# Performance work log

Measured on AMD Instinct MI355X. Metric: run time of the kernel, lower is better.

The kernel has to match this reference:

```python
import jax, jax.numpy as jnp
import numpy as np

# Dimensions (match init_kwargs / input_specs)
NF, NLOC, NALL = 1, 1024, 2048
N_DIM, E_DIM, A_DIM = 128, 16, 64
NNEI, A_SEL, AXIS = 120, 20, 4

act = jax.nn.silu


def _lin(key, i, o):
    k1, k2 = jax.random.split(key)
    w = jax.random.normal(k1, (i, o), jnp.float32) / np.float32(np.sqrt(i))
    b = jax.random.normal(k2, (o,), jnp.float32) * 0.01
    return w, b


def setup_inputs() -> dict:
    key = jax.random.key(0)
    ks = jax.random.split(key, 16)
    d = {}
    d["node_ebd_ext"] = jax.random.normal(ks[0], (NF, NALL, N_DIM), jnp.float32)
    d["edge_ebd"] = jax.random.normal(ks[1], (NF, NLOC, NNEI, E_DIM), jnp.float32)
    d["h2"] = jax.random.normal(ks[2], (NF, NLOC, NNEI, 3), jnp.float32)
    d["angle_ebd"] = jax.random.normal(ks[3], (NF, NLOC, A_SEL, A_SEL, A_DIM), jnp.float32)
    d["sw"] = jax.random.uniform(ks[4], (NF, NLOC, NNEI), jnp.float32)
    d["a_sw"] = jax.random.uniform(ks[5], (NF, NLOC, A_SEL), jnp.float32)
    d["nlist"] = jax.random.randint(ks[6], (NF, NLOC, NNEI), 0, NALL)
    d["nlist_mask"] = jnp.ones((NF, NLOC, NNEI), bool)
    d["a_nlist_mask"] = jnp.ones((NF, NLOC, A_SEL), bool)
    edge_info_dim = 2 * N_DIM + E_DIM          # 272
    angle_dim = A_DIM + N_DIM + 2 * E_DIM      # 224 (a_compress_rate == 0)
    d["w_node_self"], d["b_node_self"] = _lin(ks[7], N_DIM, N_DIM)
    d["w_node_sym"], d["b_node_sym"] = _lin(ks[8], (N_DIM + E_DIM) * AXIS, N_DIM)
    d["w_node_edge"], d["b_node_edge"] = _lin(ks[9], edge_info_dim, N_DIM)
    d["w_edge_self"], d["b_edge_self"] = _lin(ks[10], edge_info_dim, E_DIM)
    d["w_ea1"], d["b_ea1"] = _lin(ks[11], angle_dim, E_DIM)
    d["w_ea2"], d["b_ea2"] = _lin(ks[12], E_DIM, E_DIM)
    d["w_angle_self"], d["b_angle_self"] = _lin(ks[13], angle_dim, A_DIM)
    # res_residual update style: one learnable residual scale per update branch,
    # init 'const' with update_residual = 0.1
    d["n_res"] = jnp.full((3, N_DIM), 0.1, jnp.float32)  # self, sym, edge-message
    d["e_res"] = jnp.full((2, E_DIM), 0.1, jnp.float32)  # self, angle-message
    d["a_res"] = jnp.full((1, A_DIM), 0.1, jnp.float32)  # self
    return d


def _forward(node_ebd_ext, edge_ebd, h2, angle_ebd, sw, a_sw,
             w_node_self, b_node_self, w_node_sym, b_node_sym,
             w_node_edge, b_node_edge, w_edge_self, b_edge_self,
             w_ea1, b_ea1, w_ea2, b_ea2, w_angle_self, b_angle_self,
             n_res, e_res, a_res, nlist, nlist_mask, a_nlist_mask):
    nf, nall, n_dim = node_ebd_ext.shape
    _, nloc, nnei, e_dim = edge_ebd.shape
    a_sel = angle_ebd.shape[2]
    node_ebd = node_ebd_ext[:, :nloc]

    # gather neighbor node embeddings: nf x nloc x nnei x n_dim
    nei_node = jax.vmap(lambda tbl, idx: tbl[idx])(node_ebd_ext, nlist)
    nei_node = jnp.where(nlist_mask[..., None], nei_node, 0.0)

    # 1) node self update
    node_self_update = act(node_ebd @ w_node_self + b_node_self)

    # 2) node symmetrization update (grrg over both edge and neighbor-node features)
    wgt = (sw * nlist_mask)[..., None]

    def sym(ebd):
        e = ebd * wgt
        hg = jnp.einsum('flni,flnd->flid', h2, e) / np.float32(nnei)  # f,l,3,d
        grrg = jnp.einsum('flid,flia->flda', hg, hg[..., :AXIS]) / np.float32(3.0)
        return grrg.reshape(nf, nloc, -1)

    node_sym_in = jnp.concatenate([sym(nei_node), sym(edge_ebd)], axis=-1)
    node_sym_update = act(node_sym_in @ w_node_sym + b_node_sym)

    # 3) edge info = [node_i, node_j, edge_ij]
    node_i = jnp.broadcast_to(node_ebd[:, :, None, :], (nf, nloc, nnei, n_dim))
    edge_info = jnp.concatenate([node_i, nei_node, edge_ebd], axis=-1)

    # 3a) node <- edge message (sw-weighted mean over neighbors)
    node_edge_update = act(edge_info @ w_node_edge + b_node_edge) * sw[..., None]
    node_edge_update = node_edge_update.sum(axis=-2) / np.float32(nnei)

    node_new = (node_ebd + n_res[0] * node_self_update
                + n_res[1] * node_sym_update + n_res[2] * node_edge_update)

    # 4) edge self update
    edge_self_update = act(edge_info @ w_edge_self + b_edge_self)

    # 5) angle branch (a_compress_rate == 0)
    edge_for_angle = jnp.where(a_nlist_mask[..., None], edge_ebd[:, :, :a_sel, :], 0.0)
    node_angle = jnp.broadcast_to(node_ebd[:, :, None, None, :], (nf, nloc, a_sel, a_sel, n_dim))
    e_ik = jnp.broadcast_to(edge_for_angle[:, :, :, None, :], (nf, nloc, a_sel, a_sel, e_dim))
    e_ij = jnp.broadcast_to(edge_for_angle[:, :, None, :, :], (nf, nloc, a_sel, a_sel, e_dim))
    angle_info = jnp.concatenate([angle_ebd, node_angle, e_ik, e_ij], axis=-1)

    # edge <- angle message: sw-weighted reduce over one angle axis
    ea = act(angle_info @ w_ea1 + b_ea1)  # nf,nloc,a_sel,a_sel,e_dim
    weighted = a_sw[:, :, :, None, None] * a_sw[:, :, None, :, None] * ea
    reduced = weighted.sum(axis=-2) / np.float32(np.sqrt(a_sel))  # nf,nloc,a_sel,e_dim
    pad = jnp.zeros((nf, nloc, nnei - a_sel, e_dim), edge_ebd.dtype)
    padded = jnp.concatenate([reduced, pad], axis=2)
    full_mask = jnp.concatenate(
        [a_nlist_mask, jnp.zeros((nf, nloc, nnei - a_sel), bool)], axis=-1)
    # smooth_edge_update = False: keep original edge ebd where angle mask is off
    padded = jnp.where(full_mask[..., None], padded, edge_ebd)
    edge_angle_update = act(padded @ w_ea2 + b_ea2)

    edge_new = edge_ebd + e_res[0] * edge_self_update + e_res[1] * edge_angle_update

    # angle self update
    angle_self_update = act(angle_info @ w_angle_self + b_angle_self)
    angle_new = angle_ebd + a_res[0] * angle_self_update

    return node_new, edge_new, angle_new


def reference(node_ebd_ext, edge_ebd, h2, angle_ebd, sw, a_sw, nlist, nlist_mask,
              a_nlist_mask, w_node_self, b_node_self, w_node_sym, b_node_sym,
              w_node_edge, b_node_edge, w_edge_self, b_edge_self, w_ea1, b_ea1,
              w_ea2, b_ea2, w_angle_self, b_angle_self, n_res, e_res, a_res):
    return _forward(node_ebd_ext, edge_ebd, h2, angle_ebd, sw, a_sw,
                    w_node_self, b_node_self, w_node_sym, b_node_sym,
                    w_node_edge, b_node_edge, w_edge_self, b_edge_self,
                    w_ea1, b_ea1, w_ea2, b_ea2, w_angle_self, b_angle_self,
                    n_res, e_res, a_res, nlist, nlist_mask, a_nlist_mask)
```

## Files before the change

### kernel.cpp

```cpp
#include <hip/hip_runtime.h>
#include <math.h>

#define NLOC 1024
#define NALL 2048
#define NDIM 128
#define EDIM 16
#define ADIM 64
#define NNEI 120
#define ASEL 20


__device__ __forceinline__ float silu(float x) {
    return x * __builtin_amdgcn_rcpf(1.f + __expf(-x));
}

__device__ __forceinline__ unsigned short f2bf(float f) {
    unsigned int u = __float_as_uint(f);
    u += 0x7fffu + ((u >> 16) & 1u);
    return (unsigned short)(u >> 16);
}

typedef __attribute__((ext_vector_type(8))) short bf16x8;
typedef __attribute__((ext_vector_type(4))) float f32x4;

__global__ __launch_bounds__(256) void k_prep(
    const float* __restrict__ node_ext,
    const float* __restrict__ w_ne, const float* __restrict__ b_ne,
    const float* __restrict__ w_es, const float* __restrict__ b_es,
    const float* __restrict__ w_ea1, const float* __restrict__ b_ea1,
    const float* __restrict__ w_as, const float* __restrict__ b_as,
    float* __restrict__ proj, float* __restrict__ pre_e,
    float* __restrict__ pre_a, unsigned short* __restrict__ wtb)
{
    const int b = blockIdx.x, t = threadIdx.x;
    if (b == 3072) {
        for (int idx = t; idx < 64 * 80; idx += 256) {
            int k = idx / 80, o = idx - k * 80;
            float v = (o < 16) ? w_ea1[k * 16 + o] : w_as[k * 64 + (o - 16)];
            wtb[o * 64 + k] = f2bf(v);
        }
        return;
    }
    __shared__ float x[128];
    const int row = (b < 2048) ? b : (b - 2048);
    if (t < 128) x[t] = node_ext[row * 128 + t];
    __syncthreads();
    if (b < 2048) {
        if (t < 144) {
            float acc = 0.f;
            if (t < 128) {
                for (int k = 0; k < 128; k++) acc += x[k] * w_ne[(128 + k) * 128 + t];
            } else {
                int o = t - 128;
                for (int k = 0; k < 128; k++) acc += x[k] * w_es[(128 + k) * 16 + o];
            }
            proj[b * 144 + t] = acc;
        }
    } else {
        int i = b - 2048;
        if (t < 144) {
            float acc;
            if (t < 128) {
                acc = b_ne[t];
                for (int k = 0; k < 128; k++) acc += x[k] * w_ne[k * 128 + t];
            } else {
                int o = t - 128;
                acc = b_es[o];
                for (int k = 0; k < 128; k++) acc += x[k] * w_es[k * 16 + o];
            }
            pre_e[i * 144 + t] = acc;
        } else if (t < 224) {
            int o = t - 144;
            float acc;
            if (o < 16) {
                acc = b_ea1[o];
                for (int k = 0; k < 128; k++) acc += x[k] * w_ea1[(64 + k) * 16 + o];
            } else {
                int o2 = o - 16;
                acc = b_as[o2];
                for (int k = 0; k < 128; k++) acc += x[k] * w_as[(64 + k) * 64 + o2];
            }
            pre_a[i * 80 + o] = acc;
        }
    }
}

__global__ __launch_bounds__(256, 4) void k_angle(
    const float* __restrict__ angle, const float* __restrict__ edge,
    const float* __restrict__ asw,
    const float* __restrict__ w_ea1, const float* __restrict__ w_as,
    const unsigned short* __restrict__ wtb, const float* __restrict__ pre_a,
    const float* __restrict__ a_res,
    float* __restrict__ out_angle, float* __restrict__ reduced)
{
    const int i = blockIdx.x, t = threadIdx.x;
    const int lane = t & 63, wv = t >> 6;
    const int m = lane & 15, q = lane >> 4;

    __shared__ float eca_s[ASEL * 80], ecb_s[ASEL * 80], edge20_s[ASEL * EDIM];
    __shared__ float asw_s[ASEL], ares_s[ADIM], red_s[ASEL * 16];

    bf16x8 bfrag[5][2];
    #pragma unroll
    for (int nt = 0; nt < 5; nt++)
        #pragma unroll
        for (int ks = 0; ks < 2; ks++)
            bfrag[nt][ks] = *(const bf16x8*)&wtb[(nt * 16 + m) * 64 + ks * 32 + q * 8];

    for (int idx = t; idx < ASEL * EDIM; idx += 256)
        edge20_s[idx] = edge[(size_t)i * NNEI * EDIM + idx];
    if (t < ASEL) asw_s[t] = asw[i * ASEL + t];
    if (t < ADIM) ares_s[t] = a_res[t];
    for (int idx = t; idx < ASEL * 16; idx += 256) red_s[idx] = 0.f;
    __syncthreads();

    int mt = wv;
    float4 c0, c1, c2, c3;
    {
        const float* Arow = angle + ((size_t)i * 400 + mt * 16 + m) * 64 + q * 8;
        c0 = *(const float4*)(Arow + 0);
        c1 = *(const float4*)(Arow + 4);
        c2 = *(const float4*)(Arow + 32);
        c3 = *(const float4*)(Arow + 36);
    }

    for (int idx = t; idx < 2 * ASEL * 80; idx += 256) {
        int half = idx / 1600, rem = idx - half * 1600;
        int aa = rem / 80, o = rem - aa * 80;
        float acc = (half == 0) ? pre_a[i * 80 + o] : 0.f;
        if (o < 16) {
            const float* w = w_ea1 + (192 + half * 16) * 16 + o;
            #pragma unroll
            for (int k = 0; k < 16; k++) acc += edge20_s[aa * 16 + k] * w[k * 16];
        } else {
            const float* w = w_as + (192 + half * 16) * 64 + (o - 16);
            #pragma unroll
            for (int k = 0; k < 16; k++) acc += edge20_s[aa * 16 + k] * w[k * 64];
        }
        if (half == 0) eca_s[rem] = acc; else ecb_s[rem] = acc;
    }
    __syncthreads();

    for (; mt < 25; mt += 4) {
        const int nmt = mt + 4;
        float4 n0{}, n1{}, n2{}, n3{};
        if (nmt < 25) {
            const float* Arow = angle + ((size_t)i * 400 + nmt * 16 + m) * 64 + q * 8;
            n0 = *(const float4*)(Arow + 0);
            n1 = *(const float4*)(Arow + 4);
            n2 = *(const float4*)(Arow + 32);
            n3 = *(const float4*)(Arow + 36);
        }

        bf16x8 af0, af1;
        af0[0] = (short)f2bf(c0.x); af0[1] = (short)f2bf(c0.y);
        af0[2] = (short)f2bf(c0.z); af0[3] = (short)f2bf(c0.w);
        af0[4] = (short)f2bf(c1.x); af0[5] = (short)f2bf(c1.y);
        af0[6] = (short)f2bf(c1.z); af0[7] = (short)f2bf(c1.w);
        af1[0] = (short)f2bf(c2.x); af1[1] = (short)f2bf(c2.y);
        af1[2] = (short)f2bf(c2.z); af1[3] = (short)f2bf(c2.w);
        af1[4] = (short)f2bf(c3.x); af1[5] = (short)f2bf(c3.y);
        af1[6] = (short)f2bf(c3.z); af1[7] = (short)f2bf(c3.w);

        const int p0 = mt * 16 + q * 4;
        float rez[4][4];
        #pragma unroll
        for (int r = 0; r < 4; r++) {
            const float* ar = angle + ((size_t)i * 400 + p0 + r) * 64 + m - 16;
            #pragma unroll
            for (int nt = 1; nt < 5; nt++) rez[r][nt - 1] = ar[nt * 16];
        }

        f32x4 acc[5];
        #pragma unroll
        for (int nt = 0; nt < 5; nt++) {
            acc[nt] = (f32x4){0.f, 0.f, 0.f, 0.f};
            acc[nt] = __builtin_amdgcn_mfma_f32_16x16x32_bf16(af0, bfrag[nt][0], acc[nt], 0, 0, 0);
            acc[nt] = __builtin_amdgcn_mfma_f32_16x16x32_bf16(af1, bfrag[nt][1], acc[nt], 0, 0, 0);
        }

        #pragma unroll
        for (int r = 0; r < 4; r++) {
            const int p = p0 + r;
            const int a = p / 20;
            const int bb = p - a * 20;
            {
                const float s = acc[0][r] + eca_s[a * 80 + m] + ecb_s[bb * 80 + m];
                atomicAdd(&red_s[a * 16 + m], asw_s[bb] * silu(s));
            }
            const size_t base = ((size_t)i * 400 + p) * 64;
            #pragma unroll
            for (int nt = 1; nt < 5; nt++) {
                const int o = nt * 16 + m;
                const float s = acc[nt][r] + eca_s[a * 80 + o] + ecb_s[bb * 80 + o];
                out_angle[base + o - 16] = rez[r][nt - 1] + ares_s[o - 16] * silu(s);
            }
        }

        c0 = n0; c1 = n1; c2 = n2; c3 = n3;
    }
    __syncthreads();

    for (int idx = t; idx < ASEL * 16; idx += 256) {
        const int aa = idx >> 4;
        reduced[i * 320 + idx] = red_s[idx] * asw_s[aa] * 0.22360679774997896f;
    }
}

__global__ __launch_bounds__(256) void k_edge(
    const float* __restrict__ edge, const float* __restrict__ sw,
    const int* __restrict__ nlist,
    const float* __restrict__ w_ne, const float* __restrict__ w_es,
    const float* __restrict__ w_ea2, const float* __restrict__ b_ea2,
    const float* __restrict__ e_res,
    const float* __restrict__ proj, const float* __restrict__ pre_e,
    const float* __restrict__ reduced,
    float* __restrict__ neu, float* __restrict__ out_edge)
{
    const int i = blockIdx.x, t = threadIdx.x;
    __shared__ float red_s[320], esu_s[120 * 17], pre_e_s[144];
    __shared__ float wea2_s[256], bea2_s[16], eres_s[32], sw_s[120];
    __shared__ float wes_s[256];
    __shared__ float edge_s[120 * 17];
    __shared__ int nl_s[120];

    for (int idx = t; idx < 320; idx += 256) red_s[idx] = reduced[i * 320 + idx];
    for (int idx = t; idx < 1920; idx += 256) {
        const int j = idx >> 4, k = idx & 15;
        edge_s[j * 17 + k] = edge[(size_t)i * 1920 + idx];
    }
    if (t < 144) pre_e_s[t] = pre_e[i * 144 + t];
    if (t < 120) { nl_s[t] = nlist[i * 120 + t]; sw_s[t] = sw[i * 120 + t]; }
    if (t < 256) wea2_s[t] = w_ea2[t];
    if (t < 16) bea2_s[t] = b_ea2[t];
    if (t < 32) eres_s[t] = e_res[t];
    if (t >= 128 && t < 128 + 256) ;
    for (int idx = t; idx < 256; idx += 256) wes_s[idx] = w_es[256 * 16 + idx];
    __syncthreads();

    if (t < 128) {
        const int o = t;
        float w3c[16];
        #pragma unroll
        for (int k = 0; k < 16; k++) w3c[k] = w_ne[(256 + k) * 128 + o];
        const float pe = pre_e_s[o];
        float pj = proj[(size_t)nl_s[0] * 144 + o];
        float acc = 0.f;
        for (int j = 0; j < 120; j++) {
            float pn = 0.f;
            if (j + 1 < 120) pn = proj[(size_t)nl_s[j + 1] * 144 + o];
            const float* er = &edge_s[j * 17];
            float s = pe + pj;
            #pragma unroll
            for (int k = 0; k < 16; k++) s += er[k] * w3c[k];
            acc += silu(s) * sw_s[j];
            pj = pn;
        }
        neu[i * 128 + o] = acc * (1.f / 120.f);
    } else if (t < 248) {
        const int j = t - 128;
        const int n = nl_s[j];
        float pv[16];
        #pragma unroll
        for (int oo = 0; oo < 16; oo++)
            pv[oo] = pre_e_s[128 + oo] + proj[(size_t)n * 144 + 128 + oo];
        float e[16];
        #pragma unroll
        for (int k = 0; k < 16; k++) e[k] = edge_s[j * 17 + k];
        #pragma unroll 1
        for (int oo = 0; oo < 16; oo++) {
            float s = pv[oo];
            #pragma unroll
            for (int k = 0; k < 16; k++) s += e[k] * wes_s[k * 16 + oo];
            esu_s[j * 17 + oo] = silu(s);
        }
    }
    __syncthreads();

    for (int idx = t; idx < 1920; idx += 256) {
        const int j = idx >> 4, o = idx & 15;
        float s = bea2_s[o];
        if (j < 20) {
            #pragma unroll
            for (int k = 0; k < 16; k++) s += red_s[j * 16 + k] * wea2_s[k * 16 + o];
        } else {
            const float* er = &edge_s[j * 17];
            #pragma unroll
            for (int k = 0; k < 16; k++) s += er[k] * wea2_s[k * 16 + o];
        }
        const float eau = silu(s);
        const float ev = edge_s[j * 17 + o];
        out_edge[((size_t)i * 120 + j) * 16 + o] =
            ev + eres_s[o] * esu_s[j * 17 + o] + eres_s[16 + o] * eau;
    }
}

__global__ __launch_bounds__(256) void k_node(
    const float* __restrict__ node_ext, const float* __restrict__ edge,
    const float* __restrict__ h2, const float* __restrict__ sw,
    const int* __restrict__ nlist,
    const float* __restrict__ w_ns, const float* __restrict__ b_ns,
    const float* __restrict__ w_sym, const float* __restrict__ b_sym,
    const float* __restrict__ n_res, const float* __restrict__ neu,
    float* __restrict__ out_node)
{
    const int i = blockIdx.x, t = threadIdx.x;
    __shared__ float node_s[128], hjc_s[120 * 4], hgN_s[3 * 128], hgE_s[3 * 16], sym_s[576];
    __shared__ int nl_s[120];

    if (t < 128) node_s[t] = node_ext[i * 128 + t];
    if (t < 120) {
        nl_s[t] = nlist[i * 120 + t];
        const float s = sw[i * 120 + t];
        hjc_s[t * 4 + 0] = h2[((size_t)i * 120 + t) * 3 + 0] * s;
        hjc_s[t * 4 + 1] = h2[((size_t)i * 120 + t) * 3 + 1] * s;
        hjc_s[t * 4 + 2] = h2[((size_t)i * 120 + t) * 3 + 2] * s;
        hjc_s[t * 4 + 3] = 0.f;
    }
    __syncthreads();

    if (t < 128) {
        const int d = t;
        float a0 = 0.f, a1 = 0.f, a2 = 0.f;
        float v = node_ext[(size_t)nl_s[0] * 128 + d];
        for (int j = 0; j < 120; j++) {
            float vn = 0.f;
            if (j + 1 < 120) vn = node_ext[(size_t)nl_s[j + 1] * 128 + d];
            const float4 hc = *(const float4*)&hjc_s[j * 4];
            a0 += hc.x * v; a1 += hc.y * v; a2 += hc.z * v;
            v = vn;
        }
        hgN_s[0 * 128 + d] = a0 * (1.f / 120.f);
        hgN_s[1 * 128 + d] = a1 * (1.f / 120.f);
        hgN_s[2 * 128 + d] = a2 * (1.f / 120.f);
    } else if (t < 144) {
        const int d = t - 128;
        float a0 = 0.f, a1 = 0.f, a2 = 0.f;
        float v = edge[((size_t)i * 120 + 0) * 16 + d];
        for (int j = 0; j < 120; j++) {
            float vn = 0.f;
            if (j + 1 < 120) vn = edge[((size_t)i * 120 + j + 1) * 16 + d];
            const float4 hc = *(const float4*)&hjc_s[j * 4];
            a0 += hc.x * v; a1 += hc.y * v; a2 += hc.z * v;
            v = vn;
        }
        hgE_s[0 * 16 + d] = a0 * (1.f / 120.f);
        hgE_s[1 * 16 + d] = a1 * (1.f / 120.f);
        hgE_s[2 * 16 + d] = a2 * (1.f / 120.f);
    }
    __syncthreads();

    for (int idx = t; idx < 576; idx += 256) {
        if (idx < 512) {
            const int d = idx >> 2, a = idx & 3;
            sym_s[idx] = (hgN_s[d] * hgN_s[a] + hgN_s[128 + d] * hgN_s[128 + a] +
                          hgN_s[256 + d] * hgN_s[256 + a]) * (1.f / 3.f);
        } else {
            const int r = idx - 512, d = r >> 2, a = r & 3;
            sym_s[idx] = (hgE_s[d] * hgE_s[a] + hgE_s[16 + d] * hgE_s[16 + a] +
                          hgE_s[32 + d] * hgE_s[32 + a]) * (1.f / 3.f);
        }
    }
    __syncthreads();

    if (t < 128) {
        const int o = t;
        float s1 = b_ns[o];
        for (int k = 0; k < 128; k++) s1 += node_s[k] * w_ns[k * 128 + o];
        const float nsu = silu(s1);
        float s2 = b_sym[o];
        for (int k = 0; k < 576; k++) s2 += sym_s[k] * w_sym[k * 128 + o];
        const float nsy = silu(s2);
        out_node[i * 128 + o] = node_s[o] + n_res[o] * nsu + n_res[128 + o] * nsy +
                                n_res[256 + o] * neu[i * 128 + o];
    }
}

extern "C" void kernel_launch(void* const* d_in, const int* in_sizes, int n_in,
                              void* d_out, int out_size, void* d_ws, size_t ws_size,
                              hipStream_t stream)
{
    const float* node_ext = (const float*)d_in[0];
    const float* edge     = (const float*)d_in[1];
    const float* h2       = (const float*)d_in[2];
    const float* angle    = (const float*)d_in[3];
    const float* sw       = (const float*)d_in[4];
    const float* asw      = (const float*)d_in[5];
    const int*   nlist    = (const int*)d_in[6];
    const float* w_ns  = (const float*)d_in[9];  const float* b_ns  = (const float*)d_in[10];
    const float* w_sym = (const float*)d_in[11]; const float* b_sym = (const float*)d_in[12];
    const float* w_ne  = (const float*)d_in[13]; const float* b_ne  = (const float*)d_in[14];
    const float* w_es  = (const float*)d_in[15]; const float* b_es  = (const float*)d_in[16];
    const float* w_ea1 = (const float*)d_in[17]; const float* b_ea1 = (const float*)d_in[18];
    const float* w_ea2 = (const float*)d_in[19]; const float* b_ea2 = (const float*)d_in[20];
    const float* w_as  = (const float*)d_in[21]; const float* b_as  = (const float*)d_in[22];
    const float* n_res = (const float*)d_in[23];
    const float* e_res = (const float*)d_in[24];
    const float* a_res = (const float*)d_in[25];

    float* out_node  = (float*)d_out;
    float* out_edge  = out_node + (size_t)NLOC * NDIM;
    float* out_angle = out_edge + (size_t)NLOC * NNEI * EDIM;

    float* ws      = (float*)d_ws;
    float* proj    = ws;
    float* pre_e   = proj + 2048 * 144;
    float* pre_a   = pre_e + 1024 * 144;
    float* reduced = pre_a + 1024 * 80;
    float* neu     = reduced + 1024 * 320;
    unsigned short* wtb = (unsigned short*)(neu + 1024 * 128);

    k_prep<<<dim3(3073), dim3(256), 0, stream>>>(node_ext, w_ne, b_ne, w_es, b_es,
                                                 w_ea1, b_ea1, w_as, b_as,
                                                 proj, pre_e, pre_a, wtb);
    k_angle<<<dim3(1024), dim3(256), 0, stream>>>(angle, edge, asw, w_ea1, w_as,
                                                  wtb, pre_a, a_res, out_angle, reduced);
    k_edge<<<dim3(1024), dim3(256), 0, stream>>>(edge, sw, nlist, w_ne, w_es,
                                                 w_ea2, b_ea2, e_res, proj, pre_e,
                                                 reduced, neu, out_edge);
    k_node<<<dim3(1024), dim3(256), 0, stream>>>(node_ext, edge, h2, sw, nlist,
                                                 w_ns, b_ns, w_sym, b_sym, n_res,
                                                 neu, out_node);
}
```

Measured before the change: 373.6 us.

## Split angle rows across two blocks and use all threads in edge/node kernels

k_angle now launches two blocks per atom, each handling half of the 25 row tiles and writing its own slice of the reduced output. Occupancy is raised to 8 blocks per CU through launch bounds. k_edge and k_node previously left half the threads idle in long serial neighbor loops. They now split those loops across both thread halves (and eight chunks for the edge projection) and combine partial sums in shared memory. The symmetric matmul in k_node is likewise split across the two halves. The cost is duplicated eca/ecb setup in each angle block, extra shared memory and barriers, and possible register pressure from the tighter launch bounds.

```diff
diff --git a/kernel.cpp b/kernel.cpp
--- a/kernel.cpp
+++ b/kernel.cpp
@@ -85,7 +85,7 @@
     }
 }
 
-__global__ __launch_bounds__(256, 4) void k_angle(
+__global__ __launch_bounds__(256, 8) void k_angle(
     const float* __restrict__ angle, const float* __restrict__ edge,
     const float* __restrict__ asw,
     const float* __restrict__ w_ea1, const float* __restrict__ w_as,
@@ -93,9 +93,10 @@
     const float* __restrict__ a_res,
     float* __restrict__ out_angle, float* __restrict__ reduced)
 {
-    const int i = blockIdx.x, t = threadIdx.x;
+    const int i = blockIdx.x >> 1, h = blockIdx.x & 1, t = threadIdx.x;
     const int lane = t & 63, wv = t >> 6;
     const int m = lane & 15, q = lane >> 4;
+    const int mt_lo = h ? 15 : 0, mt_hi = h ? 25 : 15;
 
     __shared__ float eca_s[ASEL * 80], ecb_s[ASEL * 80], edge20_s[ASEL * EDIM];
     __shared__ float asw_s[ASEL], ares_s[ADIM], red_s[ASEL * 16];
@@ -114,7 +115,7 @@
     for (int idx = t; idx < ASEL * 16; idx += 256) red_s[idx] = 0.f;
     __syncthreads();
 
-    int mt = wv;
+    int mt = mt_lo + wv;
     float4 c0, c1, c2, c3;
     {
         const float* Arow = angle + ((size_t)i * 400 + mt * 16 + m) * 64 + q * 8;
@@ -141,10 +142,10 @@
     }
     __syncthreads();
 
-    for (; mt < 25; mt += 4) {
+    for (; mt < mt_hi; mt += 4) {
         const int nmt = mt + 4;
         float4 n0{}, n1{}, n2{}, n3{};
-        if (nmt < 25) {
+        if (nmt < mt_hi) {
             const float* Arow = angle + ((size_t)i * 400 + nmt * 16 + m) * 64 + q * 8;
             n0 = *(const float4*)(Arow + 0);
             n1 = *(const float4*)(Arow + 4);
@@ -201,7 +202,8 @@
     }
     __syncthreads();
 
-    for (int idx = t; idx < ASEL * 16; idx += 256) {
+    const int lo = h ? 192 : 0, hi = h ? 320 : 192;
+    for (int idx = lo + t; idx < hi; idx += 256) {
         const int aa = idx >> 4;
         reduced[i * 320 + idx] = red_s[idx] * asw_s[aa] * 0.22360679774997896f;
     }
@@ -222,6 +224,7 @@
     __shared__ float wea2_s[256], bea2_s[16], eres_s[32], sw_s[120];
     __shared__ float wes_s[256];
     __shared__ float edge_s[120 * 17];
+    __shared__ float neu_part[2][128];
     __shared__ int nl_s[120];
 
     for (int idx = t; idx < 320; idx += 256) red_s[idx] = reduced[i * 320 + idx];
@@ -234,21 +237,21 @@
     if (t < 256) wea2_s[t] = w_ea2[t];
     if (t < 16) bea2_s[t] = b_ea2[t];
     if (t < 32) eres_s[t] = e_res[t];
-    if (t >= 128 && t < 128 + 256) ;
     for (int idx = t; idx < 256; idx += 256) wes_s[idx] = w_es[256 * 16 + idx];
     __syncthreads();
 
-    if (t < 128) {
-        const int o = t;
+    {
+        const int o = t & 127, half = t >> 7;
+        const int j0 = half * 60, j1 = j0 + 60;
         float w3c[16];
         #pragma unroll
         for (int k = 0; k < 16; k++) w3c[k] = w_ne[(256 + k) * 128 + o];
         const float pe = pre_e_s[o];
-        float pj = proj[(size_t)nl_s[0] * 144 + o];
+        float pj = proj[(size_t)nl_s[j0] * 144 + o];
         float acc = 0.f;
-        for (int j = 0; j < 120; j++) {
+        for (int j = j0; j < j1; j++) {
             float pn = 0.f;
-            if (j + 1 < 120) pn = proj[(size_t)nl_s[j + 1] * 144 + o];
+            if (j + 1 < j1) pn = proj[(size_t)nl_s[j + 1] * 144 + o];
             const float* er = &edge_s[j * 17];
             float s = pe + pj;
             #pragma unroll
@@ -256,26 +259,20 @@
             acc += silu(s) * sw_s[j];
             pj = pn;
         }
-        neu[i * 128 + o] = acc * (1.f / 120.f);
-    } else if (t < 248) {
-        const int j = t - 128;
+        neu_part[half][o] = acc;
+    }
+
+    for (int idx = t; idx < 1920; idx += 256) {
+        const int j = idx >> 4, oo = idx & 15;
         const int n = nl_s[j];
-        float pv[16];
-        #pragma unroll
-        for (int oo = 0; oo < 16; oo++)
-            pv[oo] = pre_e_s[128 + oo] + proj[(size_t)n * 144 + 128 + oo];
-        float e[16];
-        #pragma unroll
-        for (int k = 0; k < 16; k++) e[k] = edge_s[j * 17 + k];
-        #pragma unroll 1
-        for (int oo = 0; oo < 16; oo++) {
-            float s = pv[oo];
-            #pragma unroll
-            for (int k = 0; k < 16; k++) s += e[k] * wes_s[k * 16 + oo];
-            esu_s[j * 17 + oo] = silu(s);
-        }
-    }
-    __syncthreads();
+        float s = pre_e_s[128 + oo] + proj[(size_t)n * 144 + 128 + oo];
+        #pragma unroll
+        for (int k = 0; k < 16; k++) s += edge_s[j * 17 + k] * wes_s[k * 16 + oo];
+        esu_s[j * 17 + oo] = silu(s);
+    }
+    __syncthreads();
+
+    if (t < 128) neu[i * 128 + t] = (neu_part[0][t] + neu_part[1][t]) * (1.f / 120.f);
 
     for (int idx = t; idx < 1920; idx += 256) {
         const int j = idx >> 4, o = idx & 15;
@@ -306,6 +303,9 @@
 {
     const int i = blockIdx.x, t = threadIdx.x;
     __shared__ float node_s[128], hjc_s[120 * 4], hgN_s[3 * 128], hgE_s[3 * 16], sym_s[576];
+    __shared__ float hgN_part[2][3][128];
+    __shared__ float hgE_part[8][3][16];
+    __shared__ float s2_part[128];
     __shared__ int nl_s[120];
 
     if (t < 128) node_s[t] = node_ext[i * 128 + t];
@@ -319,34 +319,48 @@
     }
     __syncthreads();
 
-    if (t < 128) {
-        const int d = t;
+    {
+        const int d = t & 127, half = t >> 7;
+        const int j0 = half * 60, j1 = j0 + 60;
         float a0 = 0.f, a1 = 0.f, a2 = 0.f;
-        float v = node_ext[(size_t)nl_s[0] * 128 + d];
-        for (int j = 0; j < 120; j++) {
+        float v = node_ext[(size_t)nl_s[j0] * 128 + d];
+        for (int j = j0; j < j1; j++) {
             float vn = 0.f;
-            if (j + 1 < 120) vn = node_ext[(size_t)nl_s[j + 1] * 128 + d];
+            if (j + 1 < j1) vn = node_ext[(size_t)nl_s[j + 1] * 128 + d];
             const float4 hc = *(const float4*)&hjc_s[j * 4];
             a0 += hc.x * v; a1 += hc.y * v; a2 += hc.z * v;
             v = vn;
         }
-        hgN_s[0 * 128 + d] = a0 * (1.f / 120.f);
-        hgN_s[1 * 128 + d] = a1 * (1.f / 120.f);
-        hgN_s[2 * 128 + d] = a2 * (1.f / 120.f);
-    } else if (t < 144) {
-        const int d = t - 128;
+        hgN_part[half][0][d] = a0;
+        hgN_part[half][1][d] = a1;
+        hgN_part[half][2][d] = a2;
+    }
+
+    if (t < 128) {
+        const int d = t & 15, ch = t >> 4;
+        const int j0 = ch * 15;
         float a0 = 0.f, a1 = 0.f, a2 = 0.f;
-        float v = edge[((size_t)i * 120 + 0) * 16 + d];
-        for (int j = 0; j < 120; j++) {
-            float vn = 0.f;
-            if (j + 1 < 120) vn = edge[((size_t)i * 120 + j + 1) * 16 + d];
+        for (int j = j0; j < j0 + 15; j++) {
+            const float v = edge[((size_t)i * 120 + j) * 16 + d];
             const float4 hc = *(const float4*)&hjc_s[j * 4];
             a0 += hc.x * v; a1 += hc.y * v; a2 += hc.z * v;
-            v = vn;
-        }
-        hgE_s[0 * 16 + d] = a0 * (1.f / 120.f);
-        hgE_s[1 * 16 + d] = a1 * (1.f / 120.f);
-        hgE_s[2 * 16 + d] = a2 * (1.f / 120.f);
+        }
+        hgE_part[ch][0][d] = a0;
+        hgE_part[ch][1][d] = a1;
+        hgE_part[ch][2][d] = a2;
+    }
+    __syncthreads();
+
+    if (t < 128) {
+        hgN_s[0 * 128 + t] = (hgN_part[0][0][t] + hgN_part[1][0][t]) * (1.f / 120.f);
+        hgN_s[1 * 128 + t] = (hgN_part[0][1][t] + hgN_part[1][1][t]) * (1.f / 120.f);
+        hgN_s[2 * 128 + t] = (hgN_part[0][2][t] + hgN_part[1][2][t]) * (1.f / 120.f);
+    } else if (t < 176) {
+        const int c = (t - 128) >> 4, d = (t - 128) & 15;
+        float s = 0.f;
+        #pragma unroll
+        for (int ch = 0; ch < 8; ch++) s += hgE_part[ch][c][d];
+        hgE_s[c * 16 + d] = s * (1.f / 120.f);
     }
     __syncthreads();
 
@@ -363,16 +377,26 @@
     }
     __syncthreads();
 
+    float s1 = 0.f, s2 = 0.f;
+    {
+        const int o = t & 127, half = t >> 7;
+        if (half == 0) {
+            s1 = b_ns[o];
+            for (int k = 0; k < 128; k++) s1 += node_s[k] * w_ns[k * 128 + o];
+            s2 = b_sym[o];
+            for (int k = 0; k < 224; k++) s2 += sym_s[k] * w_sym[k * 128 + o];
+        } else {
+            for (int k = 224; k < 576; k++) s2 += sym_s[k] * w_sym[k * 128 + o];
+            s2_part[o] = s2;
+        }
+    }
+    __syncthreads();
+
     if (t < 128) {
-        const int o = t;
-        float s1 = b_ns[o];
-        for (int k = 0; k < 128; k++) s1 += node_s[k] * w_ns[k * 128 + o];
         const float nsu = silu(s1);
-        float s2 = b_sym[o];
-        for (int k = 0; k < 576; k++) s2 += sym_s[k] * w_sym[k * 128 + o];
-        const float nsy = silu(s2);
-        out_node[i * 128 + o] = node_s[o] + n_res[o] * nsu + n_res[128 + o] * nsy +
-                                n_res[256 + o] * neu[i * 128 + o];
+        const float nsy = silu(s2 + s2_part[t]);
+        out_node[i * 128 + t] = node_s[t] + n_res[t] * nsu + n_res[128 + t] * nsy +
+                                n_res[256 + t] * neu[i * 128 + t];
     }
 }
 
@@ -413,7 +437,7 @@
     k_prep<<<dim3(3073), dim3(256), 0, stream>>>(node_ext, w_ne, b_ne, w_es, b_es,
                                                  w_ea1, b_ea1, w_as, b_as,
                                                  proj, pre_e, pre_a, wtb);
-    k_angle<<<dim3(1024), dim3(256), 0, stream>>>(angle, edge, asw, w_ea1, w_as,
+    k_angle<<<dim3(2048), dim3(256), 0, stream>>>(angle, edge, asw, w_ea1, w_as,
                                                   wtb, pre_a, a_res, out_angle, reduced);
     k_edge<<<dim3(1024), dim3(256), 0, stream>>>(edge, sw, nlist, w_ne, w_es,
                                                  w_ea2, b_ea2, e_res, proj, pre_e,
```

Result: slower. 498.4 us (+33.4%).
